# Kernel optimization log

Hardware: AMD Instinct MI355X
Metric: run time of the kernel (lower is better)

## Reference

```python
import jax, jax.numpy as jnp
import numpy as np

B, T, D = 8, 512, 1024
H, DQK, DV = 16, 128, 128  # n_heads, d_qk = emb_dim//h_qk, d_v = emb_dim//h_v


def setup_inputs() -> dict:
    key = jax.random.key(0)
    ks = jax.random.split(key, 8)
    s = 0.02
    return {
        "X": jax.random.normal(ks[0], (B, T, D), jnp.float32),
        "pos_enc_k": jax.random.normal(ks[1], (T, T, DQK), jnp.float32) * s,
        "pos_enc_v": jax.random.normal(ks[2], (T, T, DV), jnp.float32) * s,
        "Wq": jax.random.normal(ks[3], (D, H * DQK), jnp.float32) * s,
        "bq": jnp.zeros((H * DQK,), jnp.float32),
        "Wk": jax.random.normal(ks[4], (D, H * DQK), jnp.float32) * s,
        "bk": jnp.zeros((H * DQK,), jnp.float32),
        "Wv": jax.random.normal(ks[5], (D, H * DV), jnp.float32) * s,
        "bv": jnp.zeros((H * DV,), jnp.float32),
        "Wp": jax.random.normal(ks[6], (H * DV, D), jnp.float32) * s,
        "bp": jnp.zeros((D,), jnp.float32),
    }


def reference(X, pos_enc_k, pos_enc_v, Wq, bq, Wk, bk, Wv, bv, Wp, bp):
    b, t, d = X.shape
    # projections -> (b, h, t, dhead)
    Q = (X @ Wq + bq).reshape(b, t, H, DQK).transpose(0, 2, 1, 3)
    K = (X @ Wk + bk).reshape(b, t, H, DQK).transpose(0, 2, 1, 3)
    V = (X @ Wv + bv).reshape(b, t, H, DV).transpose(0, 2, 1, 3)
    # content attention + relative-position key bias
    att = jnp.einsum("bhqd,bhkd->bhqk", Q, K)
    att = att + jnp.einsum("bhqd,qkd->bhqk", Q, pos_enc_k)
    att = att / jnp.sqrt(jnp.asarray(DQK, X.dtype))
    # causal mask (do_mask=True)
    causal = jnp.tril(jnp.ones((t, t), bool))
    att = jnp.where(causal[None, None], att, jnp.asarray(-jnp.inf, att.dtype))
    att = jax.nn.softmax(att, axis=-1)
    # values + relative-position value correction
    y = jnp.einsum("bhqk,bhkd->bhqd", att, V)
    y = y + jnp.einsum("bhqk,qkd->bhqd", att, pos_enc_v)
    y = y.transpose(0, 2, 1, 3).reshape(b, t, H * DV)
    return y @ Wp + bp
```

## Files before the change

### kernel.cpp

```cpp
#include <hip/hip_runtime.h>
#include <stdint.h>

#define B_  8
#define T_  512
#define D_  1024
#define H_  16
#define DH  128
#define BH  128
#define ND  2048
#define BT  4096

typedef __attribute__((ext_vector_type(8))) short          short8;
typedef __attribute__((ext_vector_type(8))) __bf16         bf16x8;
typedef __attribute__((ext_vector_type(4))) float          f32x4;
typedef __attribute__((ext_vector_type(4))) unsigned short ushort4v;

static __device__ __forceinline__ unsigned short f2bf(float f) {
  unsigned u = __builtin_bit_cast(unsigned, f);
  u += 0x7FFFu + ((u >> 16) & 1u);
  return (unsigned short)(u >> 16);
}
static __device__ __forceinline__ float bf2f(unsigned short h) {
  unsigned u = ((unsigned)h) << 16;
  return __builtin_bit_cast(float, u);
}
static __device__ __forceinline__ f32x4 mfma16(short8 a, short8 b, f32x4 c) {
  return __builtin_amdgcn_mfma_f32_16x16x32_bf16(
      __builtin_bit_cast(bf16x8, a), __builtin_bit_cast(bf16x8, b), c, 0, 0, 0);
}
static __device__ __forceinline__ void gload16(const unsigned short* g, unsigned short* l) {
  __builtin_amdgcn_global_load_lds(
      (const __attribute__((address_space(1))) void*)g,
      (__attribute__((address_space(3))) void*)l, 16, 0, 0);
}

template <int ROWS, int COLS>
static __device__ __forceinline__ void stage_gl2(unsigned short* lds,
                                                 const unsigned short* __restrict__ src,
                                                 long stride, int tid) {
  constexpr int CPR = COLS / 8;
#pragma unroll
  for (int it = 0; it < ROWS * COLS / 8 / 256; ++it) {
    int chunk = tid + it * 256;
    int r = chunk / CPR, c8 = (chunk % CPR) * 8;
    gload16(src + (long)r * stride + c8, lds + chunk * 8);
  }
}

template <int KROWS, int LDB>
static __device__ __forceinline__ void stage_cvtP(unsigned short* lds,
                                                  const float* __restrict__ src,
                                                  long stride, int tid) {
#pragma unroll
  for (int it = 0; it < KROWS / 8; ++it) {
    int chunk = tid + it * 256;
    int r = chunk >> 5, c4 = (chunk & 31) * 4;
    f32x4 v = *(const f32x4*)(src + (long)r * stride + c4);
    ushort4v o; o.x = f2bf(v.x); o.y = f2bf(v.y); o.z = f2bf(v.z); o.w = f2bf(v.w);
    *(ushort4v*)(lds + r * LDB + c4) = o;
  }
}

static __device__ __forceinline__ void stage_pv(unsigned short* lds,
                                                const float* __restrict__ src,
                                                int tid) {
#pragma unroll
  for (int it = 0; it < 8; ++it) {
    int chunk = tid + it * 256;
    int d4 = (chunk & 3) * 4 + ((chunk >> 6) & 7) * 16;
    int k  = ((chunk >> 2) & 15) + ((chunk >> 9) & 3) * 16;
    f32x4 v = *(const f32x4*)(src + (long)k * DH + d4);
    lds[(d4 + 0) * 72 + k] = f2bf(v.x);
    lds[(d4 + 1) * 72 + k] = f2bf(v.y);
    lds[(d4 + 2) * 72 + k] = f2bf(v.z);
    lds[(d4 + 3) * 72 + k] = f2bf(v.w);
  }
}

template <int MR, int NR, int LDA, int LDB, int KD>
static __device__ __forceinline__ void mfma_blk(const unsigned short* As,
                                                const unsigned short* Bs,
                                                int a0, int b0, int lrow, int lk8,
                                                f32x4 (*acc)[NR]) {
#pragma unroll
  for (int ks = 0; ks < KD; ks += 32) {
    short8 a[MR], b[NR];
#pragma unroll
    for (int i = 0; i < MR; ++i) a[i] = *(const short8*)&As[(a0 + i * 16 + lrow) * LDA + ks + lk8];
#pragma unroll
    for (int j = 0; j < NR; ++j) b[j] = *(const short8*)&Bs[(b0 + j * 16 + lrow) * LDB + ks + lk8];
#pragma unroll
    for (int i = 0; i < MR; ++i)
#pragma unroll
      for (int j = 0; j < NR; ++j) acc[i][j] = mfma16(a[i], b[j], acc[i][j]);
  }
}

#define IDS4                             \
  const int tid  = threadIdx.x;          \
  const int lane = tid & 63;             \
  const int wid  = tid >> 6;             \
  const int lrow = lane & 15;            \
  const int lk8  = (lane >> 4) * 8;      \
  const int lr4  = (lane >> 4) * 4;      \
  const int wm = wid >> 1, wn = wid & 1;

#define LTS 132
#define LTQ 68

__global__ __launch_bounds__(256) void k_cvt(const float* __restrict__ in,
                                             unsigned short* __restrict__ outp, int n4) {
  int i = blockIdx.x * 256 + threadIdx.x;
  if (i >= n4) return;
  f32x4 v = ((const f32x4*)in)[i];
  ushort4v o;
  o.x = f2bf(v.x); o.y = f2bf(v.y); o.z = f2bf(v.z); o.w = f2bf(v.w);
  ((ushort4v*)outp)[i] = o;
}

__global__ __launch_bounds__(256) void k_transcvt(const float* __restrict__ in,
                                                  unsigned short* __restrict__ outp,
                                                  int R, int C) {
  __shared__ float tile[32][33];
  int c0 = blockIdx.x * 32, r0 = blockIdx.y * 32;
  int tx = threadIdx.x & 31, ty = threadIdx.x >> 5;
#pragma unroll
  for (int i = 0; i < 32; i += 8)
    tile[ty + i][tx] = in[(long)(r0 + ty + i) * C + (c0 + tx)];
  __syncthreads();
#pragma unroll
  for (int i = 0; i < 32; i += 8)
    outp[(long)(c0 + ty + i) * R + (r0 + tx)] = f2bf(tile[tx][ty + i]);
}

__global__ __launch_bounds__(256) void k_vtrans(const unsigned short* __restrict__ vin,
                                                unsigned short* __restrict__ vout) {
  __shared__ unsigned short tile[32][33];
  int bh = blockIdx.z;
  int t0 = blockIdx.x * 32, d0 = blockIdx.y * 32;
  int tx = threadIdx.x & 31, ty = threadIdx.x >> 5;
#pragma unroll
  for (int i = 0; i < 32; i += 8)
    tile[ty + i][tx] = vin[((long)bh * T_ + t0 + ty + i) * DH + (d0 + tx)];
  __syncthreads();
#pragma unroll
  for (int i = 0; i < 32; i += 8)
    vout[((long)bh * DH + (d0 + ty + i)) * T_ + (t0 + tx)] = tile[tx][ty + i];
}

__global__ __launch_bounds__(512, 1) void k_proj8(const unsigned short* __restrict__ Xb,
                                                  const unsigned short* __restrict__ WT,
                                                  const float* __restrict__ bq,
                                                  const float* __restrict__ bk,
                                                  const float* __restrict__ bv,
                                                  unsigned short* __restrict__ Qb,
                                                  unsigned short* __restrict__ Kb,
                                                  unsigned short* __restrict__ Vb) {
  __shared__ unsigned short lds[3 * 24576];
  const int tid  = threadIdx.x;
  const int lane = tid & 63;
  const int wid  = tid >> 6;
  const int wm   = wid >> 2;
  const int wn   = wid & 3;
  const int lrow = lane & 15;
  const int lr4  = (lane >> 4) * 4;

  const int flat = blockIdx.x, xcd = flat & 7, local = flat >> 3;
  const int mt = (xcd & 1) * 16 + (local & 15);
  const int nt = (xcd >> 1) * 6 + (local >> 4);
  const int m0 = mt * 128, n0 = nt * 256;

  const unsigned short* Asrc = Xb + (long)m0 * D_;
  const unsigned short* Bsrc = WT + (long)n0 * D_;

  auto stage = [&](int t) {
    unsigned short* base = lds + (t % 3) * 24576;
    const unsigned short* as = Asrc + t * 64;
    const unsigned short* bs = Bsrc + t * 64;
#pragma unroll
    for (int it = 0; it < 2; ++it) {
      int n = tid + it * 512;
      int r = n >> 3, c = (n & 7) ^ (r & 7);
      gload16(as + (long)r * D_ + c * 8, base + n * 8);
    }
#pragma unroll
    for (int it = 0; it < 4; ++it) {
      int n = tid + it * 512;
      int r = n >> 3, c = (n & 7) ^ (r & 7);
      gload16(bs + (long)r * D_ + c * 8, base + 8192 + n * 8);
    }
  };

  stage(0);
  stage(1);

  f32x4 acc[4][4] = {};
  for (int t = 0; t < 16; ++t) {
    if (t < 14) asm volatile("s_waitcnt vmcnt(6)" ::: "memory");
    else        asm volatile("s_waitcnt vmcnt(0)" ::: "memory");
    __builtin_amdgcn_sched_barrier(0);
    __builtin_amdgcn_s_barrier();
    __builtin_amdgcn_sched_barrier(0);
    if (t < 14) stage(t + 2);
    const unsigned short* At = lds + (t % 3) * 24576;
    const unsigned short* Bt = At + 8192;
    short8 a[4][2], b[4][2];
#pragma unroll
    for (int i = 0; i < 4; ++i) {
      int ra = wm * 64 + i * 16 + lrow;
#pragma unroll
      for (int ks = 0; ks < 2; ++ks) {
        int c = (ks * 4 + (lane >> 4)) ^ (ra & 7);
        a[i][ks] = *(const short8*)&At[ra * 64 + c * 8];
      }
    }
#pragma unroll
    for (int j = 0; j < 4; ++j) {
      int rb = wn * 64 + j * 16 + lrow;
#pragma unroll
      for (int ks = 0; ks < 2; ++ks) {
        int c = (ks * 4 + (lane >> 4)) ^ (rb & 7);
        b[j][ks] = *(const short8*)&Bt[rb * 64 + c * 8];
      }
    }
    __builtin_amdgcn_s_setprio(1);
#pragma unroll
    for (int ks = 0; ks < 2; ++ks)
#pragma unroll
      for (int i = 0; i < 4; ++i)
#pragma unroll
        for (int j = 0; j < 4; ++j)
          acc[i][j] = mfma16(a[i][ks], b[j][ks], acc[i][j]);
    __builtin_amdgcn_s_setprio(0);
  }

  const int nb = n0 >> 11;
  const float* biasp = nb == 0 ? bq : (nb == 1 ? bk : bv);
  unsigned short* dst = nb == 0 ? Qb : (nb == 1 ? Kb : Vb);
#pragma unroll
  for (int i = 0; i < 4; ++i)
#pragma unroll
    for (int j = 0; j < 4; ++j) {
      int c = (n0 & 2047) + wn * 64 + j * 16 + lrow;
      int h = c >> 7, dd = c & 127;
      float bias = biasp[c];
#pragma unroll
      for (int r = 0; r < 4; ++r) {
        int m = m0 + wm * 64 + i * 16 + lr4 + r;
        int bb = m >> 9, tt = m & (T_ - 1);
        dst[((long)(bb * H_ + h) * T_ + tt) * DH + dd] = f2bf(acc[i][j][r] + bias);
      }
    }
}

__global__ __launch_bounds__(256) void k_posk(const unsigned short* __restrict__ Qb,
                                              const float* __restrict__ Pk,
                                              unsigned short* __restrict__ att) {
  const int bid = blockIdx.x;
  const int q = (bid & 1) ? (T_ - 1 - (bid >> 1)) : (bid >> 1);
  const int ktiles = (q >> 6) + 1;
  __shared__ unsigned short As[128 * 128], Bs[64 * 136];
  IDS4
  stage_gl2<128, 128>(As, Qb + (long)q * DH, (long)T_ * DH, tid);
  for (int kt = 0; kt < ktiles; ++kt) {
    stage_cvtP<64, 136>(Bs, Pk + ((long)q * T_ + kt * 64) * DH, DH, tid);
    __syncthreads();
    f32x4 acc[4][2] = {};
    mfma_blk<4, 2, 128, 136, 128>(As, Bs, wm * 64, wn * 32, lrow, lk8, acc);
#pragma unroll
    for (int i = 0; i < 4; ++i)
#pragma unroll
      for (int j = 0; j < 2; ++j) {
        int k = kt * 64 + wn * 32 + j * 16 + lrow;
#pragma unroll
        for (int r = 0; r < 4; ++r) {
          int bh = wm * 64 + i * 16 + lr4 + r;
          att[((long)q * BH + bh) * T_ + k] = f2bf(acc[i][j][r]);
        }
      }
    __syncthreads();
  }
}

__global__ __launch_bounds__(256) void k_qkv(const unsigned short* __restrict__ Qb,
                                             const unsigned short* __restrict__ Kb,
                                             const unsigned short* __restrict__ Vt,
                                             unsigned short* __restrict__ att,
                                             float* __restrict__ Sinv,
                                             unsigned short* __restrict__ Ybb) {
  const int bh = blockIdx.x & 127, pr = blockIdx.x >> 7;
  __shared__ unsigned short Qs[64 * 128], Ks[64 * 128], Vs[128 * 64];
  __shared__ unsigned short Ps[64 * 72];
  __shared__ float lt[64 * LTQ];
  __shared__ float sInv[64];
  const int tid = threadIdx.x;
  const int lane = tid & 63, wid = tid >> 6;
  const int wm = wid >> 1, wn = wid & 1;
  const int lrow = lane & 15, lk8 = (lane >> 4) * 8, lr4 = (lane >> 4) * 4;
  const int row = tid >> 2, c0 = (tid & 3) * 16;
  const float scale = 0.08838834764831845f;
  const int b = bh >> 4, h = bh & 15;

  for (int pass = 0; pass < 2; ++pass) {
    const int qt = pass ? 7 - pr : pr;
    const int q0 = qt * 64, ktiles = qt + 1;
    const int qabs = q0 + row;
    unsigned short* arow = att + ((long)qabs * BH + bh) * T_;
    {
      const unsigned short* src = Qb + ((long)bh * T_ + q0) * DH;
#pragma unroll
      for (int it = 0; it < 4; ++it) {
        int n = tid + it * 256;
        int r = n >> 4, c = (n & 15) ^ (r & 7);
        gload16(src + (long)r * DH + c * 8, Qs + n * 8);
      }
    }
    float ssum = 0.f;
    f32x4 accv[2][4] = {};
    for (int kt = 0; kt < ktiles; ++kt) {
      const unsigned short* ksrc = Kb + ((long)bh * T_ + kt * 64) * DH;
#pragma unroll
      for (int it = 0; it < 4; ++it) {
        int n = tid + it * 256;
        int r = n >> 4, c = (n & 15) ^ (r & 7);
        gload16(ksrc + (long)r * DH + c * 8, Ks + n * 8);
      }
      const unsigned short* vsrc = Vt + (long)bh * DH * T_ + kt * 64;
#pragma unroll
      for (int it = 0; it < 4; ++it) {
        int n = tid + it * 256;
        int r = n >> 3, c = (n & 7) ^ (r & 7);
        gload16(vsrc + (long)r * T_ + c * 8, Vs + n * 8);
      }
      short8 pb0 = *(const short8*)(arow + kt * 64 + c0);
      short8 pb1 = *(const short8*)(arow + kt * 64 + c0 + 8);
      __syncthreads();
      f32x4 acc[2][2] = {};
#pragma unroll
      for (int ks = 0; ks < 4; ++ks) {
        short8 aq[2], bk2[2];
#pragma unroll
        for (int i = 0; i < 2; ++i) {
          int ra = wm * 32 + i * 16 + lrow;
          int c = (ks * 4 + (lane >> 4)) ^ (ra & 7);
          aq[i] = *(const short8*)&Qs[ra * 128 + c * 8];
        }
#pragma unroll
        for (int j = 0; j < 2; ++j) {
          int rb = wn * 32 + j * 16 + lrow;
          int c = (ks * 4 + (lane >> 4)) ^ (rb & 7);
          bk2[j] = *(const short8*)&Ks[rb * 128 + c * 8];
        }
#pragma unroll
        for (int i = 0; i < 2; ++i)
#pragma unroll
          for (int j = 0; j < 2; ++j)
            acc[i][j] = mfma16(aq[i], bk2[j], acc[i][j]);
      }
#pragma unroll
      for (int i = 0; i < 2; ++i)
#pragma unroll
        for (int j = 0; j < 2; ++j)
#pragma unroll
          for (int r = 0; r < 4; ++r)
            lt[(wm * 32 + i * 16 + lr4 + r) * LTQ + wn * 32 + j * 16 + lrow] = acc[i][j][r];
      __syncthreads();
      short8 o0, o1;
#pragma unroll
      for (int jj = 0; jj < 8; ++jj) {
        int k = kt * 64 + c0 + jj;
        float e0 = (k <= qabs)
                   ? __expf((lt[row * LTQ + c0 + jj] + bf2f((unsigned short)pb0[jj])) * scale) : 0.f;
        float e1 = (k + 8 <= qabs)
                   ? __expf((lt[row * LTQ + c0 + 8 + jj] + bf2f((unsigned short)pb1[jj])) * scale) : 0.f;
        o0[jj] = (short)f2bf(e0);
        o1[jj] = (short)f2bf(e1);
        ssum += e0 + e1;
      }
      *(short8*)(arow + kt * 64 + c0) = o0;
      *(short8*)(arow + kt * 64 + c0 + 8) = o1;
      *(short8*)&Ps[row * 72 + c0] = o0;
      *(short8*)&Ps[row * 72 + c0 + 8] = o1;
      __syncthreads();
#pragma unroll
      for (int ks = 0; ks < 2; ++ks) {
        short8 ap[2], bv2[4];
#pragma unroll
        for (int i = 0; i < 2; ++i) {
          int ra = wm * 32 + i * 16 + lrow;
          ap[i] = *(const short8*)&Ps[ra * 72 + ks * 32 + lk8];
        }
#pragma unroll
        for (int j = 0; j < 4; ++j) {
          int rb = wn * 64 + j * 16 + lrow;
          int c = ((ks * 4) + (lane >> 4)) ^ (rb & 7);
          bv2[j] = *(const short8*)&Vs[rb * 64 + c * 8];
        }
#pragma unroll
        for (int i = 0; i < 2; ++i)
#pragma unroll
          for (int j = 0; j < 4; ++j)
            accv[i][j] = mfma16(ap[i], bv2[j], accv[i][j]);
      }
      __syncthreads();
    }
    ssum += __shfl_xor(ssum, 1, 64);
    ssum += __shfl_xor(ssum, 2, 64);
    float si = 1.f / ssum;
    if ((tid & 3) == 0) { sInv[row] = si; Sinv[(long)qabs * BH + bh] = si; }
    __syncthreads();
#pragma unroll
    for (int i = 0; i < 2; ++i) {
      float sc2[4];
#pragma unroll
      for (int r = 0; r < 4; ++r) sc2[r] = sInv[wm * 32 + i * 16 + lr4 + r];
#pragma unroll
      for (int j = 0; j < 4; ++j) {
        int d = wn * 64 + j * 16 + lrow;
#pragma unroll
        for (int r = 0; r < 4; ++r) {
          int q = q0 + wm * 32 + i * 16 + lr4 + r;
          Ybb[(long)(b * T_ + q) * ND + h * DH + d] = f2bf(accv[i][j][r] * sc2[r]);
        }
      }
    }
    __syncthreads();
  }
}

__global__ __launch_bounds__(256) void k_posv(const unsigned short* __restrict__ P,
                                              const float* __restrict__ Pv,
                                              const float* __restrict__ Sinv,
                                              unsigned short* __restrict__ Ybb) {
  const int bid = blockIdx.x;
  const int q = (bid & 1) ? (T_ - 1 - (bid >> 1)) : (bid >> 1);
  const int ktiles = (q >> 6) + 1;
  __shared__ unsigned short As[128 * 64], Bs[128 * 72];
  __shared__ float lt[64 * LTQ];
  IDS4
  f32x4 acc[4][4] = {};
  for (int kt = 0; kt < ktiles; ++kt) {
    stage_gl2<128, 64>(As, P + (long)q * BH * T_ + kt * 64, T_, tid);
    stage_pv(Bs, Pv + ((long)q * T_ + kt * 64) * DH, tid);
    __syncthreads();
    mfma_blk<4, 4, 64, 72, 64>(As, Bs, wm * 64, wn * 64, lrow, lk8, acc);
    __syncthreads();
  }
  const int row = tid >> 2, c0 = (tid & 3) * 16;
#pragma unroll
  for (int hb = 0; hb < 2; ++hb)
#pragma unroll
    for (int hd = 0; hd < 2; ++hd) {
      int bh = hb * 64 + row;
      long idx = ((long)((bh >> 4) * T_ + q)) * ND + (bh & 15) * DH + hd * 64 + c0;
      short8 y0 = *(const short8*)&Ybb[idx];
      short8 y1 = *(const short8*)&Ybb[idx + 8];
      float sc = Sinv[(long)q * BH + bh];
      if (wm == hb && wn == hd) {
#pragma unroll
        for (int i = 0; i < 4; ++i)
#pragma unroll
          for (int j = 0; j < 4; ++j)
#pragma unroll
            for (int r = 0; r < 4; ++r)
              lt[(i * 16 + lr4 + r) * LTQ + j * 16 + lrow] = acc[i][j][r];
      }
      __syncthreads();
      short8 o0, o1;
#pragma unroll
      for (int jj = 0; jj < 8; ++jj) {
        o0[jj] = (short)f2bf(lt[row * LTQ + c0 + jj] * sc + bf2f((unsigned short)y0[jj]));
        o1[jj] = (short)f2bf(lt[row * LTQ + c0 + 8 + jj] * sc + bf2f((unsigned short)y1[jj]));
      }
      *(short8*)&Ybb[idx] = o0;
      *(short8*)&Ybb[idx + 8] = o1;
      __syncthreads();
    }
}

__global__ __launch_bounds__(256) void k_oproj(const unsigned short* __restrict__ Ybb,
                                               const unsigned short* __restrict__ WpT,
                                               const float* __restrict__ bp,
                                               float* __restrict__ outp) {
  __shared__ unsigned short As[128 * 64], Bs[128 * 64];
  IDS4
  const int m0 = blockIdx.y * 128, n0 = blockIdx.x * 128;
  f32x4 acc[4][4] = {};
  for (int kk = 0; kk < ND; kk += 64) {
    stage_gl2<128, 64>(As, Ybb + (long)m0 * ND + kk, ND, tid);
    stage_gl2<128, 64>(Bs, WpT + (long)n0 * ND + kk, ND, tid);
    __syncthreads();
    mfma_blk<4, 4, 64, 64, 64>(As, Bs, wm * 64, wn * 64, lrow, lk8, acc);
    __syncthreads();
  }
  float* lt = (float*)As;
  const int row = tid >> 4, c8 = (tid & 15) * 8;
  f32x4 b0 = *(const f32x4*)(bp + n0 + c8);
  f32x4 b1 = *(const f32x4*)(bp + n0 + c8 + 4);
#pragma unroll
  for (int rr = 0; rr < 8; ++rr) {
    if (wm == (rr >> 2)) {
      const int ii = rr & 3;
#pragma unroll
      for (int j = 0; j < 4; ++j)
#pragma unroll
        for (int r = 0; r < 4; ++r)
          lt[(lr4 + r) * LTS + wn * 64 + j * 16 + lrow] = acc[ii][j][r];
    }
    __syncthreads();
    f32x4 v0 = *(const f32x4*)&lt[row * LTS + c8];
    f32x4 v1 = *(const f32x4*)&lt[row * LTS + c8 + 4];
    int m = m0 + rr * 16 + row;
    v0.x += b0.x; v0.y += b0.y; v0.z += b0.z; v0.w += b0.w;
    v1.x += b1.x; v1.y += b1.y; v1.z += b1.z; v1.w += b1.w;
    *(f32x4*)&outp[(long)m * D_ + n0 + c8] = v0;
    *(f32x4*)&outp[(long)m * D_ + n0 + c8 + 4] = v1;
    __syncthreads();
  }
}

extern "C" void kernel_launch(void* const* d_in, const int* in_sizes, int n_in,
                              void* d_out, int out_size, void* d_ws, size_t ws_size,
                              hipStream_t stream) {
  const float* X  = (const float*)d_in[0];
  const float* Pk = (const float*)d_in[1];
  const float* Pv = (const float*)d_in[2];
  const float* Wq = (const float*)d_in[3];
  const float* bq = (const float*)d_in[4];
  const float* Wk = (const float*)d_in[5];
  const float* bk = (const float*)d_in[6];
  const float* Wv = (const float*)d_in[7];
  const float* bv = (const float*)d_in[8];
  const float* Wp = (const float*)d_in[9];
  const float* bp = (const float*)d_in[10];
  float* out = (float*)d_out;

  uint8_t* w = (uint8_t*)d_ws;
  unsigned short* Xb  = (unsigned short*)w; w += (size_t)BT * D_ * 2;
  unsigned short* WT  = (unsigned short*)w; w += (size_t)3 * ND * D_ * 2;
  unsigned short* WpT = (unsigned short*)w; w += (size_t)D_ * ND * 2;
  unsigned short* Qb  = (unsigned short*)w; w += (size_t)BH * T_ * DH * 2;
  unsigned short* Kb  = (unsigned short*)w; w += (size_t)BH * T_ * DH * 2;
  unsigned short* Vb  = (unsigned short*)w; w += (size_t)BH * T_ * DH * 2;
  unsigned short* Vt  = (unsigned short*)w; w += (size_t)BH * DH * T_ * 2;
  unsigned short* att = (unsigned short*)w; w += (size_t)T_ * BH * T_ * 2;
  unsigned short* Ybb = (unsigned short*)w; w += (size_t)BT * ND * 2;
  float*          Sinv= (float*)w;          w += (size_t)T_ * BH * 4;

  k_cvt<<<BT * D_ / 4 / 256, 256, 0, stream>>>(X, Xb, BT * D_ / 4);
  k_transcvt<<<dim3(ND / 32, D_ / 32), 256, 0, stream>>>(Wq, WT, D_, ND);
  k_transcvt<<<dim3(ND / 32, D_ / 32), 256, 0, stream>>>(Wk, WT + (size_t)ND * D_, D_, ND);
  k_transcvt<<<dim3(ND / 32, D_ / 32), 256, 0, stream>>>(Wv, WT + (size_t)2 * ND * D_, D_, ND);
  k_transcvt<<<dim3(D_ / 32, ND / 32), 256, 0, stream>>>(Wp, WpT, ND, D_);
  k_proj8<<<768, 512, 0, stream>>>(Xb, WT, bq, bk, bv, Qb, Kb, Vb);
  k_vtrans<<<dim3(T_ / 32, DH / 32, BH), 256, 0, stream>>>(Vb, Vt);
  k_posk<<<T_, 256, 0, stream>>>(Qb, Pk, att);
  k_qkv<<<512, 256, 0, stream>>>(Qb, Kb, Vt, att, Sinv, Ybb);
  k_posv<<<T_, 256, 0, stream>>>(att, Pv, Sinv, Ybb);
  k_oproj<<<dim3(D_ / 128, BT / 128), 256, 0, stream>>>(Ybb, WpT, bp, out);
}
```

Measured before the change: 252.5 us.

## Software-pipeline fp32 positional-encoding loads and split GEMM staging across half-tiles

The QKV projection GEMM now issues its A and B tile prefetches separately, one in each half of the K-step, with an extra barrier between the halves. This spreads global-load issue around the MFMA work. The posk and posv kernels double-buffer their converted positional-encoding tiles: the next tile's fp32 loads go into registers before the MFMAs, and the bf16 conversion and LDS write happen after them. This hides global load latency behind compute, at the cost of more registers, more LDS and extra barriers. The vmcnt wait thresholds in the GEMM were changed, and the new A/B stage split may not match the vmcnt(6) accounting, so the synchronisation is fragile.

After: 254.1 us. Within noise of the previous version (+0.6%).

```diff
diff --git a/kernel.cpp b/kernel.cpp
--- a/kernel.cpp
+++ b/kernel.cpp
@@ -44,36 +44,6 @@
     int chunk = tid + it * 256;
     int r = chunk / CPR, c8 = (chunk % CPR) * 8;
     gload16(src + (long)r * stride + c8, lds + chunk * 8);
-  }
-}
-
-template <int KROWS, int LDB>
-static __device__ __forceinline__ void stage_cvtP(unsigned short* lds,
-                                                  const float* __restrict__ src,
-                                                  long stride, int tid) {
-#pragma unroll
-  for (int it = 0; it < KROWS / 8; ++it) {
-    int chunk = tid + it * 256;
-    int r = chunk >> 5, c4 = (chunk & 31) * 4;
-    f32x4 v = *(const f32x4*)(src + (long)r * stride + c4);
-    ushort4v o; o.x = f2bf(v.x); o.y = f2bf(v.y); o.z = f2bf(v.z); o.w = f2bf(v.w);
-    *(ushort4v*)(lds + r * LDB + c4) = o;
-  }
-}
-
-static __device__ __forceinline__ void stage_pv(unsigned short* lds,
-                                                const float* __restrict__ src,
-                                                int tid) {
-#pragma unroll
-  for (int it = 0; it < 8; ++it) {
-    int chunk = tid + it * 256;
-    int d4 = (chunk & 3) * 4 + ((chunk >> 6) & 7) * 16;
-    int k  = ((chunk >> 2) & 15) + ((chunk >> 9) & 3) * 16;
-    f32x4 v = *(const f32x4*)(src + (long)k * DH + d4);
-    lds[(d4 + 0) * 72 + k] = f2bf(v.x);
-    lds[(d4 + 1) * 72 + k] = f2bf(v.y);
-    lds[(d4 + 2) * 72 + k] = f2bf(v.z);
-    lds[(d4 + 3) * 72 + k] = f2bf(v.w);
   }
 }
 
@@ -173,65 +143,87 @@
   const unsigned short* Asrc = Xb + (long)m0 * D_;
   const unsigned short* Bsrc = WT + (long)n0 * D_;
 
-  auto stage = [&](int t) {
+  auto stageA = [&](int t) {
     unsigned short* base = lds + (t % 3) * 24576;
     const unsigned short* as = Asrc + t * 64;
-    const unsigned short* bs = Bsrc + t * 64;
 #pragma unroll
     for (int it = 0; it < 2; ++it) {
       int n = tid + it * 512;
       int r = n >> 3, c = (n & 7) ^ (r & 7);
       gload16(as + (long)r * D_ + c * 8, base + n * 8);
     }
+  };
+  auto stageB = [&](int t) {
+    unsigned short* base = lds + (t % 3) * 24576 + 8192;
+    const unsigned short* bs = Bsrc + t * 64;
 #pragma unroll
     for (int it = 0; it < 4; ++it) {
       int n = tid + it * 512;
       int r = n >> 3, c = (n & 7) ^ (r & 7);
-      gload16(bs + (long)r * D_ + c * 8, base + 8192 + n * 8);
+      gload16(bs + (long)r * D_ + c * 8, base + 8192 + n * 8 - 8192);
     }
   };
 
-  stage(0);
-  stage(1);
+  stageA(0); stageB(0);
+  stageA(1); stageB(1);
 
   f32x4 acc[4][4] = {};
   for (int t = 0; t < 16; ++t) {
-    if (t < 14) asm volatile("s_waitcnt vmcnt(6)" ::: "memory");
+    if (t < 15) asm volatile("s_waitcnt vmcnt(6)" ::: "memory");
     else        asm volatile("s_waitcnt vmcnt(0)" ::: "memory");
     __builtin_amdgcn_sched_barrier(0);
     __builtin_amdgcn_s_barrier();
     __builtin_amdgcn_sched_barrier(0);
-    if (t < 14) stage(t + 2);
     const unsigned short* At = lds + (t % 3) * 24576;
     const unsigned short* Bt = At + 8192;
-    short8 a[4][2], b[4][2];
-#pragma unroll
-    for (int i = 0; i < 4; ++i) {
-      int ra = wm * 64 + i * 16 + lrow;
-#pragma unroll
-      for (int ks = 0; ks < 2; ++ks) {
-        int c = (ks * 4 + (lane >> 4)) ^ (ra & 7);
-        a[i][ks] = *(const short8*)&At[ra * 64 + c * 8];
-      }
-    }
-#pragma unroll
-    for (int j = 0; j < 4; ++j) {
-      int rb = wn * 64 + j * 16 + lrow;
-#pragma unroll
-      for (int ks = 0; ks < 2; ++ks) {
-        int c = (ks * 4 + (lane >> 4)) ^ (rb & 7);
-        b[j][ks] = *(const short8*)&Bt[rb * 64 + c * 8];
-      }
-    }
-    __builtin_amdgcn_s_setprio(1);
-#pragma unroll
-    for (int ks = 0; ks < 2; ++ks)
+    {
+      short8 a[4], b[4];
+#pragma unroll
+      for (int i = 0; i < 4; ++i) {
+        int ra = wm * 64 + i * 16 + lrow;
+        int c = (lane >> 4) ^ (ra & 7);
+        a[i] = *(const short8*)&At[ra * 64 + c * 8];
+      }
+#pragma unroll
+      for (int j = 0; j < 4; ++j) {
+        int rb = wn * 64 + j * 16 + lrow;
+        int c = (lane >> 4) ^ (rb & 7);
+        b[j] = *(const short8*)&Bt[rb * 64 + c * 8];
+      }
+      if (t < 14) stageA(t + 2);
+      __builtin_amdgcn_s_setprio(1);
 #pragma unroll
       for (int i = 0; i < 4; ++i)
 #pragma unroll
         for (int j = 0; j < 4; ++j)
-          acc[i][j] = mfma16(a[i][ks], b[j][ks], acc[i][j]);
-    __builtin_amdgcn_s_setprio(0);
+          acc[i][j] = mfma16(a[i], b[j], acc[i][j]);
+      __builtin_amdgcn_s_setprio(0);
+    }
+    __builtin_amdgcn_s_barrier();
+    __builtin_amdgcn_sched_barrier(0);
+    {
+      short8 a[4], b[4];
+#pragma unroll
+      for (int i = 0; i < 4; ++i) {
+        int ra = wm * 64 + i * 16 + lrow;
+        int c = (4 + (lane >> 4)) ^ (ra & 7);
+        a[i] = *(const short8*)&At[ra * 64 + c * 8];
+      }
+#pragma unroll
+      for (int j = 0; j < 4; ++j) {
+        int rb = wn * 64 + j * 16 + lrow;
+        int c = (4 + (lane >> 4)) ^ (rb & 7);
+        b[j] = *(const short8*)&Bt[rb * 64 + c * 8];
+      }
+      if (t < 14) stageB(t + 2);
+      __builtin_amdgcn_s_setprio(1);
+#pragma unroll
+      for (int i = 0; i < 4; ++i)
+#pragma unroll
+        for (int j = 0; j < 4; ++j)
+          acc[i][j] = mfma16(a[i], b[j], acc[i][j]);
+      __builtin_amdgcn_s_setprio(0);
+    }
   }
 
   const int nb = n0 >> 11;
@@ -259,14 +251,44 @@
   const int bid = blockIdx.x;
   const int q = (bid & 1) ? (T_ - 1 - (bid >> 1)) : (bid >> 1);
   const int ktiles = (q >> 6) + 1;
-  __shared__ unsigned short As[128 * 128], Bs[64 * 136];
+  __shared__ unsigned short As[128 * 128];
+  __shared__ unsigned short Bs[2][64 * 136];
   IDS4
   stage_gl2<128, 128>(As, Qb + (long)q * DH, (long)T_ * DH, tid);
+  f32x4 pv[8];
+  const float* psrc = Pk + (long)q * T_ * DH;
+  auto loadPk = [&](int kt) {
+#pragma unroll
+    for (int it = 0; it < 8; ++it) {
+      int chunk = tid + it * 256;
+      int r = chunk >> 5, c4 = (chunk & 31) * 4;
+      pv[it] = *(const f32x4*)(psrc + (long)(kt * 64 + r) * DH + c4);
+    }
+  };
+  auto writeB = [&](int buf) {
+#pragma unroll
+    for (int it = 0; it < 8; ++it) {
+      int chunk = tid + it * 256;
+      int r = chunk >> 5, c4 = (chunk & 31) * 4;
+      ushort4v o;
+      o.x = f2bf(pv[it].x); o.y = f2bf(pv[it].y); o.z = f2bf(pv[it].z); o.w = f2bf(pv[it].w);
+      *(ushort4v*)&Bs[buf][r * 136 + c4] = o;
+    }
+  };
+  loadPk(0);
+  asm volatile("s_waitcnt vmcnt(0)" ::: "memory");
+  writeB(0);
+  asm volatile("s_waitcnt lgkmcnt(0)" ::: "memory");
+  __builtin_amdgcn_s_barrier();
   for (int kt = 0; kt < ktiles; ++kt) {
-    stage_cvtP<64, 136>(Bs, Pk + ((long)q * T_ + kt * 64) * DH, DH, tid);
-    __syncthreads();
+    const bool pre = (kt + 1 < ktiles);
+    if (pre) loadPk(kt + 1);
     f32x4 acc[4][2] = {};
-    mfma_blk<4, 2, 128, 136, 128>(As, Bs, wm * 64, wn * 32, lrow, lk8, acc);
+    mfma_blk<4, 2, 128, 136, 128>(As, Bs[kt & 1], wm * 64, wn * 32, lrow, lk8, acc);
+    if (pre) {
+      asm volatile("s_waitcnt vmcnt(0)" ::: "memory");
+      writeB((kt + 1) & 1);
+    }
 #pragma unroll
     for (int i = 0; i < 4; ++i)
 #pragma unroll
@@ -278,7 +300,8 @@
           att[((long)q * BH + bh) * T_ + k] = f2bf(acc[i][j][r]);
         }
       }
-    __syncthreads();
+    asm volatile("s_waitcnt lgkmcnt(0)" ::: "memory");
+    __builtin_amdgcn_s_barrier();
   }
 }
 
@@ -435,16 +458,53 @@
   const int bid = blockIdx.x;
   const int q = (bid & 1) ? (T_ - 1 - (bid >> 1)) : (bid >> 1);
   const int ktiles = (q >> 6) + 1;
-  __shared__ unsigned short As[128 * 64], Bs[128 * 72];
+  __shared__ unsigned short As[128 * 64];
+  __shared__ unsigned short Bs[2][128 * 72];
   __shared__ float lt[64 * LTQ];
   IDS4
+  f32x4 pv[8];
+  const float* psrc = Pv + (long)q * T_ * DH;
+  auto loadPv = [&](int kt) {
+#pragma unroll
+    for (int it = 0; it < 8; ++it) {
+      int chunk = tid + it * 256;
+      int d4 = (chunk & 3) * 4 + ((chunk >> 6) & 7) * 16;
+      int k  = ((chunk >> 2) & 15) + ((chunk >> 9) & 3) * 16;
+      pv[it] = *(const f32x4*)(psrc + (long)(kt * 64 + k) * DH + d4);
+    }
+  };
+  auto writeB = [&](int buf) {
+#pragma unroll
+    for (int it = 0; it < 8; ++it) {
+      int chunk = tid + it * 256;
+      int d4 = (chunk & 3) * 4 + ((chunk >> 6) & 7) * 16;
+      int k  = ((chunk >> 2) & 15) + ((chunk >> 9) & 3) * 16;
+      Bs[buf][(d4 + 0) * 72 + k] = f2bf(pv[it].x);
+      Bs[buf][(d4 + 1) * 72 + k] = f2bf(pv[it].y);
+      Bs[buf][(d4 + 2) * 72 + k] = f2bf(pv[it].z);
+      Bs[buf][(d4 + 3) * 72 + k] = f2bf(pv[it].w);
+    }
+  };
+  loadPv(0);
+  asm volatile("s_waitcnt vmcnt(0)" ::: "memory");
+  writeB(0);
+  asm volatile("s_waitcnt lgkmcnt(0)" ::: "memory");
+  __builtin_amdgcn_s_barrier();
   f32x4 acc[4][4] = {};
   for (int kt = 0; kt < ktiles; ++kt) {
+    const bool pre = (kt + 1 < ktiles);
     stage_gl2<128, 64>(As, P + (long)q * BH * T_ + kt * 64, T_, tid);
-    stage_pv(Bs, Pv + ((long)q * T_ + kt * 64) * DH, tid);
-    __syncthreads();
-    mfma_blk<4, 4, 64, 72, 64>(As, Bs, wm * 64, wn * 64, lrow, lk8, acc);
-    __syncthreads();
+    if (pre) loadPv(kt + 1);
+    if (pre) asm volatile("s_waitcnt vmcnt(8)" ::: "memory");
+    else     asm volatile("s_waitcnt vmcnt(0)" ::: "memory");
+    __builtin_amdgcn_s_barrier();
+    mfma_blk<4, 4, 64, 72, 64>(As, Bs[kt & 1], wm * 64, wn * 64, lrow, lk8, acc);
+    if (pre) {
+      asm volatile("s_waitcnt vmcnt(0)" ::: "memory");
+      writeB((kt + 1) & 1);
+    }
+    asm volatile("s_waitcnt lgkmcnt(0)" ::: "memory");
+    __builtin_amdgcn_s_barrier();
   }
   const int row = tid >> 2, c0 = (tid & 3) * 16;
 #pragma unroll
```
